# Optimization experiments

Hardware: AMD Instinct MI355X
Metric: run time of the kernel (lower is better)

## Reference

```python
import jax, jax.numpy as jnp
import numpy as np

N, D, E, H = 100000, 128, 1600000, 256  # nodes, feat dim, edges, backbone hidden
EPS = 1e-5
NEG_SLOPE = 0.01


def setup_inputs() -> dict:
    key = jax.random.key(0)
    ks = jax.random.split(key, 16)
    s = 0.02
    return {
        "x": jax.random.normal(ks[0], (N, D), dtype=jnp.float32),
        "edges": jax.random.randint(ks[1], (2, E), 0, N, dtype=jnp.int64),
        # merge layer: Linear(2D -> D)
        "W_merge": jax.random.normal(ks[2], (2 * D, D), dtype=jnp.float32) * s,
        "b_merge": jnp.zeros((D,), dtype=jnp.float32),
        # GRUCell(D, D): weights stored torch-style (3D, D)
        "W_ih": jax.random.normal(ks[3], (3 * D, D), dtype=jnp.float32) * s,
        "W_hh": jax.random.normal(ks[4], (3 * D, D), dtype=jnp.float32) * s,
        "b_ih": jnp.zeros((3 * D,), dtype=jnp.float32),
        "b_hh": jnp.zeros((3 * D,), dtype=jnp.float32),
        # backbone: Linear(D->256), BN(256), Linear(256->D), BN(D)
        "W1": jax.random.normal(ks[5], (D, H), dtype=jnp.float32) * s,
        "b1": jnp.zeros((H,), dtype=jnp.float32),
        "g1": jnp.ones((H,), dtype=jnp.float32),
        "be1": jnp.zeros((H,), dtype=jnp.float32),
        "W2": jax.random.normal(ks[6], (H, D), dtype=jnp.float32) * s,
        "b2": jnp.zeros((D,), dtype=jnp.float32),
        "g2": jnp.ones((D,), dtype=jnp.float32),
        "be2": jnp.zeros((D,), dtype=jnp.float32),
    }


def _batchnorm(y, g, b):
    m = jnp.mean(y, axis=0)
    v = jnp.var(y, axis=0)  # biased, as torch BN uses in normalization
    return g * (y - m) * jax.lax.rsqrt(v + EPS) + b


def _leaky_relu(y):
    return jnp.where(y >= 0, y, NEG_SLOPE * y)


def reference(x, edges, W_merge, b_merge, W_ih, W_hh, b_ih, b_hh,
              W1, b1, g1, be1, W2, b2, g2, be2):
    n = x.shape[0]
    src, dst = edges[0], edges[1]
    x_nbr = x[src]                                   # (E, D) gather
    agg_sum = jax.ops.segment_sum(x_nbr, dst, num_segments=n)
    agg_max = jax.ops.segment_max(x_nbr, dst, num_segments=n)
    agg_max = jnp.where(jnp.isneginf(agg_max), jnp.zeros_like(agg_max), agg_max)
    # merge 'cat' -> Linear(2D -> D)
    merged = jnp.concatenate([agg_sum, agg_max], axis=-1) @ W_merge + b_merge
    # GRUCell update: input=merged, hidden=x
    gi = merged @ W_ih.T + b_ih                      # (N, 3D)
    gh = x @ W_hh.T + b_hh                           # (N, 3D)
    i_r, i_z, i_n = jnp.split(gi, 3, axis=-1)
    h_r, h_z, h_n = jnp.split(gh, 3, axis=-1)
    r = jax.nn.sigmoid(i_r + h_r)
    z = jax.nn.sigmoid(i_z + h_z)
    nn_ = jnp.tanh(i_n + r * h_n)
    h = (1.0 - z) * nn_ + z * x
    # backbone
    y = _batchnorm(_leaky_relu(h @ W1 + b1), g1, be1)
    y = _batchnorm(_leaky_relu(y @ W2 + b2), g2, be2)
    return y
```

## Files before the change

### kernel.cpp

```cpp
#include <hip/hip_runtime.h>
#include <math.h>

#define DD 128
#define CAPB 2048
#define MAXNB 1600

typedef __attribute__((ext_vector_type(8))) short bf16x8;
typedef __attribute__((ext_vector_type(4))) float f32x4;

__device__ __forceinline__ unsigned short f2bf(float f) {
    unsigned u = __float_as_uint(f);
    unsigned r = u + 0x7FFF + ((u >> 16) & 1);
    return (unsigned short)(r >> 16);
}
__device__ __forceinline__ float bf2f(unsigned short h) {
    return __uint_as_float(((unsigned)h) << 16);
}

__device__ __forceinline__ float fsigm(float x) {
    float e = __builtin_amdgcn_exp2f(-1.442695041f * x);
    return __builtin_amdgcn_rcpf(1.0f + e);
}
__device__ __forceinline__ float ftanh(float x) {
    float e = __builtin_amdgcn_exp2f(2.885390082f * x);
    return 1.0f - 2.0f * __builtin_amdgcn_rcpf(1.0f + e);
}

__device__ __forceinline__ void gld16(const unsigned short* g, unsigned short* l) {
    __builtin_amdgcn_global_load_lds(
        (const __attribute__((address_space(1))) void*)g,
        (__attribute__((address_space(3))) void*)l, 16, 0, 0);
}

__global__ void k_wsfail(float* __restrict__ out, float val, int n) {
    int i = blockIdx.x * 256 + threadIdx.x;
    if (i < n) out[i] = (i == 0) ? val : 0.0f;
}

__global__ void k_setup(const int* __restrict__ e32, int* __restrict__ flag,
                        float* __restrict__ sums, int* __restrict__ gCur, int NB,
                        const float* __restrict__ W1, const float* __restrict__ W2,
                        unsigned short* __restrict__ w1T, unsigned short* __restrict__ w2T,
                        const float* __restrict__ x, unsigned short* __restrict__ AGG,
                        int total_x4) {
    const int bid = blockIdx.x;
    const int t = threadIdx.x;
    if (bid == 0) {
        if (t == 0) {
            int f = 1;
            for (int i = 1; i < 16; i += 2) f &= (e32[i] == 0);
            *flag = f;
        }
        for (int i = t; i < 768; i += 256) sums[i] = 0.0f;
    } else if (bid < 8) {
        int i = (bid - 1) * 256 + t;
        if (i < NB) gCur[i] = 0;
    } else if (bid < 136) {
        int i = (bid - 8) * 256 + t;
        int j = i >> 7, k = i & 127;
        w1T[j * 128 + k] = f2bf(W1[k * 256 + j]);
    } else if (bid < 264) {
        int i = (bid - 136) * 256 + t;
        int j = i >> 8, k = i & 255;
        w2T[j * 256 + k] = f2bf(W2[k * 128 + j]);
    } else {
        int idx = (bid - 264) * 256 + t;
        if (idx < total_x4) {
            int i = idx >> 5, j4 = (idx & 31) * 4;
            float4 v = *(const float4*)(x + (size_t)i * 128 + j4);
            unsigned lo = (unsigned)f2bf(v.x) | ((unsigned)f2bf(v.y) << 16);
            unsigned hi = (unsigned)f2bf(v.z) | ((unsigned)f2bf(v.w) << 16);
            unsigned short* p = AGG + (size_t)i * 384 + 256 + j4;
            *(unsigned*)(p) = lo;
            *(unsigned*)(p + 2) = hi;
        }
    }
}

__global__ void k_fusew(const float* __restrict__ Wm, const float* __restrict__ Wih,
                        const float* __restrict__ Whh, const float* __restrict__ bm,
                        const float* __restrict__ b_ih, const float* __restrict__ b_hh,
                        unsigned short* __restrict__ BtG, float* __restrict__ biasG) {
    const int j = blockIdx.x;
    const int c = threadIdx.x;
    const int g = j >> 7, d = j & 127;
    const int pj = ((d >> 4) << 6) + (g << 4) + (d & 15);
    float acc = 0.0f;
    if (j < 384) {
        const float* wr = Wih + (size_t)j * 128;
        const float* wc = Wm + (size_t)c * 128;
        for (int m = 0; m < 128; m++) acc += wc[m] * wr[m];
    }
    BtG[(size_t)pj * 384 + c] = f2bf(acc);
    if (c < 128) {
        float v = 0.0f;
        if (j < 256) v = Whh[(size_t)j * 128 + c];
        else if (j >= 384) v = Whh[(size_t)(j - 128) * 128 + c];
        BtG[(size_t)pj * 384 + 256 + c] = f2bf(v);
    }
    if (c == 0) {
        float b;
        if (j < 256) b = b_ih[j] + b_hh[j];
        else if (j < 384) b = b_ih[j];
        else b = b_hh[j - 128];
        if (j < 384) {
            const float* wr = Wih + (size_t)j * 128;
            float dd = 0.0f;
            for (int m = 0; m < 128; m++) dd += bm[m] * wr[m];
            b += dd;
        }
        biasG[pj] = b;
    }
}

__global__ __launch_bounds__(256) void k_bin(const void* __restrict__ edges_raw,
                                             const int* __restrict__ flag,
                                             int* __restrict__ gCur,
                                             unsigned* __restrict__ binned,
                                             int E, int Nn, int NB) {
    __shared__ int cnt_[MAXNB];
    __shared__ int cur_[MAXNB];
    const int t = threadIdx.x;
    const int e0 = blockIdx.x * 4096;
    for (int i = t; i < NB; i += 256) cnt_[i] = 0;
    __syncthreads();
    const int is64 = *flag;
    for (int k = 0; k < 16; k++) {
        int e = e0 + k * 256 + t;
        if (e < E) {
            int d = is64 ? (int)((const long long*)edges_raw)[(size_t)E + e]
                         : ((const int*)edges_raw)[(size_t)E + e];
            d = min(max(d, 0), Nn - 1);
            atomicAdd(&cnt_[d >> 6], 1);
        }
    }
    __syncthreads();
    for (int i = t; i < NB; i += 256) {
        int c = cnt_[i];
        cur_[i] = (c > 0) ? atomicAdd(&gCur[i], c) : 0;
    }
    __syncthreads();
    for (int k = 0; k < 16; k++) {
        int e = e0 + k * 256 + t;
        if (e < E) {
            int s, d;
            if (is64) {
                s = (int)((const long long*)edges_raw)[e];
                d = (int)((const long long*)edges_raw)[(size_t)E + e];
            } else {
                s = ((const int*)edges_raw)[e];
                d = ((const int*)edges_raw)[(size_t)E + e];
            }
            s = min(max(s, 0), Nn - 1);
            d = min(max(d, 0), Nn - 1);
            int b = d >> 6;
            int p = atomicAdd(&cur_[b], 1);
            if (p < CAPB)
                binned[(size_t)b * CAPB + p] = (unsigned)s | ((unsigned)(d & 63) << 23);
        }
    }
}

__global__ __launch_bounds__(256) void k_bagg(const unsigned* __restrict__ binned,
                                              const int* __restrict__ gCur,
                                              const void* __restrict__ edges_raw,
                                              const int* __restrict__ flag,
                                              unsigned short* __restrict__ AGG,
                                              int E, int Nn) {
    __shared__ unsigned lsrc[CAPB];
    __shared__ int deg_[64], off_[64], cur2_[64];
    __shared__ int sa[64], sb[64];
    const int t = threadIdx.x;
    const int wave = t >> 6;
    const int lane = t & 63;
    const int b = blockIdx.x;
    const int node0 = b << 6;
    const int nloc = min(64, Nn - node0);
    const int cnt = gCur[b];
    const int c2 = lane * 2;
    const unsigned c4 = (unsigned)lane * 4u;

    if (cnt <= CAPB) {
        if (t < 64) deg_[t] = 0;
        __syncthreads();
        for (int i = t; i < cnt; i += 256)
            atomicAdd(&deg_[binned[(size_t)b * CAPB + i] >> 23], 1);
        __syncthreads();
        if (t < 64) sa[t] = deg_[t];
        __syncthreads();
        for (int off = 1; off < 64; off <<= 1) {
            if (t < 64) sb[t] = sa[t] + ((t >= off) ? sa[t - off] : 0);
            __syncthreads();
            if (t < 64) sa[t] = sb[t];
            __syncthreads();
        }
        if (t < 64) {
            off_[t] = sa[t] - deg_[t];
            cur2_[t] = off_[t];
        }
        __syncthreads();
        for (int i = t; i < cnt; i += 256) {
            unsigned e = binned[(size_t)b * CAPB + i];
            int dl = e >> 23;
            int p = atomicAdd(&cur2_[dl], 1);
            lsrc[p] = (e & 0x7FFFFF) * 768u + 512u;
        }
        __syncthreads();
        const char* AGGb = (const char*)AGG;
        for (int ln = wave; ln < nloc; ln += 4) {
            const int o = off_[ln];
            const int d = deg_[ln];
            float sx = 0.f, sy = 0.f;
            float mx = -INFINITY, my = -INFINITY;
            int e = 0;
            for (; e + 7 < d; e += 8) {
                unsigned v[8];
#pragma unroll
                for (int u = 0; u < 8; u++)
                    v[u] = *(const unsigned*)(AGGb + lsrc[o + e + u] + c4);
#pragma unroll
                for (int u = 0; u < 8; u++) {
                    float lo = bf2f((unsigned short)(v[u] & 0xffff));
                    float hi = bf2f((unsigned short)(v[u] >> 16));
                    sx += lo; sy += hi;
                    mx = fmaxf(mx, lo); my = fmaxf(my, hi);
                }
            }
            for (; e + 3 < d; e += 4) {
                unsigned v[4];
#pragma unroll
                for (int u = 0; u < 4; u++)
                    v[u] = *(const unsigned*)(AGGb + lsrc[o + e + u] + c4);
#pragma unroll
                for (int u = 0; u < 4; u++) {
                    float lo = bf2f((unsigned short)(v[u] & 0xffff));
                    float hi = bf2f((unsigned short)(v[u] >> 16));
                    sx += lo; sy += hi;
                    mx = fmaxf(mx, lo); my = fmaxf(my, hi);
                }
            }
            for (; e < d; e++) {
                unsigned v0 = *(const unsigned*)(AGGb + lsrc[o + e] + c4);
                float lo = bf2f((unsigned short)(v0 & 0xffff));
                float hi = bf2f((unsigned short)(v0 >> 16));
                sx += lo; sy += hi;
                mx = fmaxf(mx, lo); my = fmaxf(my, hi);
            }
            if (d == 0) { mx = 0.f; my = 0.f; }
            unsigned short* row = AGG + (size_t)(node0 + ln) * 384;
            *(unsigned*)(row + c2) = (unsigned)f2bf(sx) | ((unsigned)f2bf(sy) << 16);
            *(unsigned*)(row + 128 + c2) = (unsigned)f2bf(mx) | ((unsigned)f2bf(my) << 16);
        }
    } else {
        const int is64 = *flag;
        for (int ln = wave; ln < nloc; ln += 4) {
            const int node = node0 + ln;
            float sx = 0.f, sy = 0.f;
            float mx = -INFINITY, my = -INFINITY;
            int d = 0;
            for (int e = 0; e < E; e++) {
                int dd = is64 ? (int)((const long long*)edges_raw)[(size_t)E + e]
                              : ((const int*)edges_raw)[(size_t)E + e];
                dd = min(max(dd, 0), Nn - 1);
                if (dd == node) {
                    int s = is64 ? (int)((const long long*)edges_raw)[e]
                                 : ((const int*)edges_raw)[e];
                    s = min(max(s, 0), Nn - 1);
                    unsigned v0 = *(const unsigned*)(AGG + (size_t)s * 384 + 256 + c2);
                    float ax = bf2f((unsigned short)(v0 & 0xffff));
                    float ay = bf2f((unsigned short)(v0 >> 16));
                    sx += ax; sy += ay;
                    mx = fmaxf(mx, ax); my = fmaxf(my, ay);
                    d++;
                }
            }
            if (d == 0) { mx = 0.f; my = 0.f; }
            unsigned short* row = AGG + (size_t)node * 384;
            *(unsigned*)(row + c2) = (unsigned)f2bf(sx) | ((unsigned)f2bf(sy) << 16);
            *(unsigned*)(row + 128 + c2) = (unsigned)f2bf(mx) | ((unsigned)f2bf(my) << 16);
        }
    }
}

template <int AFFINE, int LEAKY, int STATS, int GRUE>
__global__ __launch_bounds__(256) void k_mgemm(
    const unsigned short* __restrict__ A, int lda,
    const unsigned short* __restrict__ Bt,
    const float* __restrict__ bias,
    const float* __restrict__ sumA, const float* __restrict__ sqA,
    const float* __restrict__ gA, const float* __restrict__ beA,
    unsigned short* __restrict__ Cb, int ldc,
    int M, int K, float* __restrict__ sumO, float* __restrict__ sqO, float invN,
    const unsigned short* __restrict__ Xb) {
    __shared__ unsigned short ABs[2][2][4096];
    __shared__ float sc1[256], sh1[256];
    __shared__ float ssum[128], ssq[128];
    unsigned short* RP = &ABs[0][0][0];

    const int t = threadIdx.x;
    const int lane = t & 63;
    const int wave = t >> 6;
    const int wr = (wave >> 1) * 64;
    const int wc = (wave & 1) * 64;
    const int quad = lane >> 4;
    const int l16 = lane & 15;
    const int sig = (l16 >> 1) & 3;

    const int ncb = gridDim.x;
    const int nwg = ncb * gridDim.y;
    int lin = blockIdx.y * ncb + blockIdx.x;
    const int qq = nwg >> 3, rr = nwg & 7;
    const int xcd = lin & 7, pos = lin >> 3;
    const int nl = (xcd < rr ? xcd * (qq + 1) : rr * (qq + 1) + (xcd - rr) * qq) + pos;
    const int j0 = (nl % ncb) * 128;
    const int r0 = (nl / ncb) * 128;

    if (AFFINE) {
        float m = sumA[t] * invN;
        float v = sqA[t] * invN - m * m;
        if (v < 0.f) v = 0.f;
        float rs = rsqrtf(v + 1e-5f);
        float sc = gA[t] * rs;
        sc1[t] = sc;
        sh1[t] = beA[t] - m * sc;
    }
    if (STATS && t < 128) { ssum[t] = 0.f; ssq[t] = 0.f; }
    if (AFFINE || STATS) __syncthreads();

    f32x4 acc[4][4];
#pragma unroll
    for (int i = 0; i < 4; i++)
#pragma unroll
        for (int j = 0; j < 4; j++) acc[i][j] = (f32x4){0.f, 0.f, 0.f, 0.f};

    const int rowl = lane >> 2;
    const int gsw8 = (((lane & 3) ^ ((lane >> 3) & 3))) * 8;

    const int srow = t >> 2;
    const int sg8 = (t & 3) * 8;
    const int swz8 = (((t & 3) ^ ((t >> 3) & 3))) * 8;
    float4 areg[2];

    auto stageA = [&](int buf, int k0) {
#pragma unroll
        for (int p = 0; p < 2; p++) {
            int row = (wave * 2 + p) * 16 + rowl;
            int gr = r0 + row;
            if (gr >= M) gr = M - 1;
            gld16(A + (size_t)gr * lda + k0 + gsw8,
                  &ABs[buf][0][(wave * 2 + p) * 512]);
        }
    };
    auto stageB = [&](int buf, int k0) {
#pragma unroll
        for (int p = 0; p < 2; p++) {
            int row = (wave * 2 + p) * 16 + rowl;
            gld16(Bt + (size_t)(j0 + row) * K + k0 + gsw8,
                  &ABs[buf][1][(wave * 2 + p) * 512]);
        }
    };
    auto loadA = [&](int k0) {
#pragma unroll
        for (int p = 0; p < 2; p++) {
            int gr = r0 + p * 64 + srow;
            areg[p] = make_float4(0.f, 0.f, 0.f, 0.f);
            if (gr < M) areg[p] = *(const float4*)(A + (size_t)gr * lda + k0 + sg8);
        }
    };
    auto writeA = [&](int buf, int k0) {
        union U8 { float4 f; unsigned short u[8]; } uv;
#pragma unroll
        for (int p = 0; p < 2; p++) {
            uv.f = areg[p];
#pragma unroll
            for (int q = 0; q < 8; q++) {
                float f = bf2f(uv.u[q]) * sc1[k0 + sg8 + q] + sh1[k0 + sg8 + q];
                uv.u[q] = f2bf(f);
            }
            *(float4*)&ABs[buf][0][(p * 64 + srow) * 32 + swz8] = uv.f;
        }
    };

    if (!AFFINE) {
        stageA(0, 0); stageB(0, 0);
        if (32 < K) { stageA(1, 32); stageB(1, 32); }
        for (int k0 = 0; k0 < K; k0 += 32) {
            const int cur = (k0 >> 5) & 1;
            if (k0 + 32 < K)
                asm volatile("s_waitcnt vmcnt(4)\n\ts_barrier" ::: "memory");
            else
                asm volatile("s_waitcnt vmcnt(0)\n\ts_barrier" ::: "memory");
            bf16x8 af[4], bfr[4];
#pragma unroll
            for (int i = 0; i < 4; i++) {
                af[i]  = *(bf16x8*)&ABs[cur][0][(wr + i * 16 + l16) * 32 + (quad ^ sig) * 8];
                bfr[i] = *(bf16x8*)&ABs[cur][1][(wc + i * 16 + l16) * 32 + (quad ^ sig) * 8];
            }
            asm volatile("s_waitcnt lgkmcnt(0)\n\ts_barrier" ::: "memory");
            if (k0 + 64 < K) { stageA(cur, k0 + 64); stageB(cur, k0 + 64); }
#pragma unroll
            for (int mt = 0; mt < 4; mt++)
#pragma unroll
                for (int nt = 0; nt < 4; nt++)
                    acc[mt][nt] = __builtin_amdgcn_mfma_f32_16x16x32_bf16(
                        af[mt], bfr[nt], acc[mt][nt], 0, 0, 0);
        }
    } else {
        loadA(0); writeA(0, 0);
        stageB(0, 0);
        __syncthreads();
        int buf = 0;
        for (int k0 = 0; k0 < K; k0 += 32) {
            const int kn = k0 + 32;
            const bool hasNext = kn < K;
            if (hasNext) {
                loadA(kn);
                stageB(buf ^ 1, kn);
            }
            bf16x8 af[4], bfr[4];
#pragma unroll
            for (int i = 0; i < 4; i++) {
                af[i]  = *(bf16x8*)&ABs[buf][0][(wr + i * 16 + l16) * 32 + (quad ^ sig) * 8];
                bfr[i] = *(bf16x8*)&ABs[buf][1][(wc + i * 16 + l16) * 32 + (quad ^ sig) * 8];
            }
#pragma unroll
            for (int mt = 0; mt < 4; mt++)
#pragma unroll
                for (int nt = 0; nt < 4; nt++)
                    acc[mt][nt] = __builtin_amdgcn_mfma_f32_16x16x32_bf16(
                        af[mt], bfr[nt], acc[mt][nt], 0, 0, 0);
            if (hasNext) writeA(buf ^ 1, kn);
            __syncthreads();
            buf ^= 1;
        }
    }

    if (GRUE) {
        const int dimb = (j0 + wc) >> 2;
        const int dloc = (wc >> 2) + l16;
        const float bR = bias[j0 + wc + l16];
        const float bZ = bias[j0 + wc + 16 + l16];
        const float bI = bias[j0 + wc + 32 + l16];
        const float bH = bias[j0 + wc + 48 + l16];
#pragma unroll
        for (int mt = 0; mt < 4; mt++) {
#pragma unroll
            for (int reg = 0; reg < 4; reg++) {
                int rloc = wr + mt * 16 + quad * 4 + reg;
                int grow = r0 + rloc;
                int gi = grow < M ? grow : M - 1;
                float r = fsigm(acc[mt][0][reg] + bR);
                float z = fsigm(acc[mt][1][reg] + bZ);
                float nn = ftanh(acc[mt][2][reg] + bI + r * (acc[mt][3][reg] + bH));
                float xv = bf2f(Xb[(size_t)gi * 384 + 256 + dimb + l16]);
                float h = (1.0f - z) * nn + z * xv;
                RP[rloc * 40 + dloc] = f2bf(h);
            }
        }
        __syncthreads();
#pragma unroll
        for (int p = 0; p < 2; p++) {
            int id = p * 256 + t;
            int rloc = id >> 2, ck = id & 3;
            int grow = r0 + rloc;
            if (grow < M)
                *(float4*)(Cb + (size_t)grow * ldc + (j0 >> 2) + ck * 8) =
                    *(const float4*)&RP[rloc * 40 + ck * 8];
        }
        return;
    }

#pragma unroll
    for (int half = 0; half < 2; half++) {
        if (wr == half * 64) {
#pragma unroll
            for (int nt = 0; nt < 4; nt++) {
                int colLoc = wc + nt * 16 + l16;
                float bv = bias[j0 + colLoc];
                float s = 0.f, q = 0.f;
#pragma unroll
                for (int mt = 0; mt < 4; mt++) {
#pragma unroll
                    for (int reg = 0; reg < 4; reg++) {
                        int rloc = mt * 16 + quad * 4 + reg;
                        float v = acc[mt][nt][reg] + bv;
                        if (LEAKY) v = (v >= 0.f) ? v : 0.01f * v;
                        if (STATS && (r0 + half * 64 + rloc) < M) { s += v; q += v * v; }
                        RP[rloc * 128 + colLoc] = f2bf(v);
                    }
                }
                if (STATS) {
                    atomicAdd(&ssum[colLoc], s);
                    atomicAdd(&ssq[colLoc], q);
                }
            }
        }
        __syncthreads();
#pragma unroll
        for (int p = 0; p < 4; p++) {
            int id = p * 256 + t;
            int rloc = id >> 4;
            int ck = id & 15;
            int grow = r0 + half * 64 + rloc;
            if (grow < M)
                *(float4*)(Cb + (size_t)grow * ldc + j0 + ck * 8) =
                    *(const float4*)&RP[rloc * 128 + ck * 8];
        }
        __syncthreads();
    }
    if (STATS && t < 128) {
        atomicAdd(&sumO[j0 + t], ssum[t]);
        atomicAdd(&sqO[j0 + t], ssq[t]);
    }
}

__global__ void k_affine2(const unsigned short* __restrict__ ypre, float* __restrict__ out,
                          const float* __restrict__ sum2, const float* __restrict__ sq2,
                          const float* __restrict__ g2, const float* __restrict__ be2,
                          int total4, float invN) {
    __shared__ float sc[128], sh[128];
    int t = threadIdx.x;
    if (t < 128) {
        float m = sum2[t] * invN;
        float v = sq2[t] * invN - m * m;
        if (v < 0.f) v = 0.f;
        float rs = rsqrtf(v + 1e-5f);
        float s = g2[t] * rs;
        sc[t] = s;
        sh[t] = be2[t] - m * s;
    }
    __syncthreads();
    int idx = blockIdx.x * 256 + t;
    if (idx >= total4) return;
    int i4 = idx * 4;
    int c = i4 & 127;
    unsigned u0 = *(const unsigned*)(ypre + i4);
    unsigned u1 = *(const unsigned*)(ypre + i4 + 2);
    float4 o;
    o.x = bf2f((unsigned short)(u0 & 0xffff)) * sc[c]     + sh[c];
    o.y = bf2f((unsigned short)(u0 >> 16))    * sc[c + 1] + sh[c + 1];
    o.z = bf2f((unsigned short)(u1 & 0xffff)) * sc[c + 2] + sh[c + 2];
    o.w = bf2f((unsigned short)(u1 >> 16))    * sc[c + 3] + sh[c + 3];
    *(float4*)(out + i4) = o;
}

extern "C" void kernel_launch(void* const* d_in, const int* in_sizes, int n_in,
                              void* d_out, int out_size, void* d_ws, size_t ws_size,
                              hipStream_t stream) {
    const float* x       = (const float*)d_in[0];
    const void*  edges   = d_in[1];
    const float* W_merge = (const float*)d_in[2];
    const float* b_merge = (const float*)d_in[3];
    const float* W_ih    = (const float*)d_in[4];
    const float* W_hh    = (const float*)d_in[5];
    const float* b_ih    = (const float*)d_in[6];
    const float* b_hh    = (const float*)d_in[7];
    const float* W1      = (const float*)d_in[8];
    const float* b1      = (const float*)d_in[9];
    const float* g1      = (const float*)d_in[10];
    const float* be1     = (const float*)d_in[11];
    const float* W2      = (const float*)d_in[12];
    const float* b2      = (const float*)d_in[13];
    const float* g2      = (const float*)d_in[14];
    const float* be2     = (const float*)d_in[15];

    const int N = in_sizes[0] / DD;
    const int E = in_sizes[1] / 2;
    float* out = (float*)d_out;

    size_t need = ((size_t)640 * N + 120000) * sizeof(float);
    if (ws_size < need) {
        k_wsfail<<<(out_size + 255) / 256, 256, 0, stream>>>(
            out, (float)(ws_size >> 20), out_size);
        return;
    }

    const int NB = (N + 63) >> 6;

    float* ws = (float*)d_ws;
    unsigned short* AGG  = (unsigned short*)ws;
    unsigned short* y1b  = (unsigned short*)ws;
    unsigned short* ypre = (unsigned short*)(ws + (size_t)128 * N);
    unsigned short* hb16 = (unsigned short*)(ws + (size_t)448 * N);

    unsigned* binned = (unsigned*)(ws + (size_t)512 * N);
    int* gCur = (int*)(binned + (size_t)NB * CAPB);

    float* wbase = (float*)(gCur + NB + 64);
    unsigned short* BtG = (unsigned short*)wbase;
    unsigned short* w1T = (unsigned short*)(wbase + 98304);
    unsigned short* w2T = (unsigned short*)(wbase + 98304 + 16384);
    float* biasG = wbase + 98304 + 32768;
    float* sums  = biasG + 512;
    float* sum1 = sums, *sq1 = sums + 256, *sum2 = sums + 512, *sq2 = sums + 640;
    int*   flag  = (int*)(sums + 768);

    const int nrb  = (N + 127) / 128;
    const int ncvt4 = (N * 32 + 255) / 256;
    const float invN = 1.0f / (float)N;

    k_setup<<<264 + ncvt4, 256, 0, stream>>>(
        (const int*)edges, flag, sums, gCur, NB, W1, W2, w1T, w2T, x, AGG, N * 32);
    k_fusew<<<512, 256, 0, stream>>>(W_merge, W_ih, W_hh, b_merge, b_ih, b_hh, BtG, biasG);
    k_bin<<<(E + 4095) / 4096, 256, 0, stream>>>(edges, flag, gCur, binned, E, N, NB);
    k_bagg<<<NB, 256, 0, stream>>>(binned, gCur, edges, flag, AGG, E, N);
    k_mgemm<0, 0, 0, 1><<<dim3(4, nrb), 256, 0, stream>>>(
        AGG, 384, BtG, biasG, nullptr, nullptr, nullptr, nullptr,
        hb16, 128, N, 384, nullptr, nullptr, invN, AGG);
    k_mgemm<0, 1, 1, 0><<<dim3(2, nrb), 256, 0, stream>>>(
        hb16, 128, w1T, b1, nullptr, nullptr, nullptr, nullptr,
        y1b, 256, N, 128, sum1, sq1, invN, nullptr);
    k_mgemm<1, 1, 1, 0><<<dim3(1, nrb), 256, 0, stream>>>(
        y1b, 256, w2T, b2, sum1, sq1, g1, be1,
        ypre, 128, N, 256, sum2, sq2, invN, nullptr);
    k_affine2<<<ncvt4, 256, 0, stream>>>(ypre, out, sum2, sq2, g2, be2, N * 32, invN);
}
```

Before: 445.2 us.

## Split-edge 8-byte gathers in aggregation and dedicated 256-row GRU GEMM kernel

The aggregation kernel now has each half-wave handle alternating edges. Each lane loads 8 bytes (4 bf16 features), and the two halves are combined with a cross-half shuffle. The first half writes sums and the second half writes maxima. The fused merge/GRU GEMM moves out of the generic template into a dedicated kernel with 256-row tiles and 128 output columns per block. It uses direct-to-LDS async loads with double buffering, so each block covers two GRU dimension groups and reuses the B tile across more rows. The trade-off is higher register pressure (32 accumulators per wave) and fewer blocks, which may hurt occupancy.

```diff
diff --git a/kernel.cpp b/kernel.cpp
--- a/kernel.cpp
+++ b/kernel.cpp
@@ -177,8 +177,10 @@
     const int node0 = b << 6;
     const int nloc = min(64, Nn - node0);
     const int cnt = gCur[b];
+    const int half = lane >> 5;
+    const int hl = lane & 31;
+    const unsigned c8 = (unsigned)hl * 8u;
     const int c2 = lane * 2;
-    const unsigned c4 = (unsigned)lane * 4u;
 
     if (cnt <= CAPB) {
         if (t < 64) deg_[t] = 0;
@@ -210,46 +212,67 @@
         for (int ln = wave; ln < nloc; ln += 4) {
             const int o = off_[ln];
             const int d = deg_[ln];
-            float sx = 0.f, sy = 0.f;
-            float mx = -INFINITY, my = -INFINITY;
+            float s0 = 0.f, s1 = 0.f, s2 = 0.f, s3 = 0.f;
+            float m0 = -INFINITY, m1 = -INFINITY, m2 = -INFINITY, m3 = -INFINITY;
             int e = 0;
-            for (; e + 7 < d; e += 8) {
-                unsigned v[8];
+            for (; e + 15 < d; e += 16) {
+                uint2 v[8];
 #pragma unroll
                 for (int u = 0; u < 8; u++)
-                    v[u] = *(const unsigned*)(AGGb + lsrc[o + e + u] + c4);
+                    v[u] = *(const uint2*)(AGGb + lsrc[o + e + 2 * u + half] + c8);
 #pragma unroll
                 for (int u = 0; u < 8; u++) {
-                    float lo = bf2f((unsigned short)(v[u] & 0xffff));
-                    float hi = bf2f((unsigned short)(v[u] >> 16));
-                    sx += lo; sy += hi;
-                    mx = fmaxf(mx, lo); my = fmaxf(my, hi);
+                    float a = bf2f((unsigned short)(v[u].x & 0xffff));
+                    float bb = bf2f((unsigned short)(v[u].x >> 16));
+                    float cc = bf2f((unsigned short)(v[u].y & 0xffff));
+                    float dd2 = bf2f((unsigned short)(v[u].y >> 16));
+                    s0 += a; s1 += bb; s2 += cc; s3 += dd2;
+                    m0 = fmaxf(m0, a); m1 = fmaxf(m1, bb);
+                    m2 = fmaxf(m2, cc); m3 = fmaxf(m3, dd2);
                 }
             }
-            for (; e + 3 < d; e += 4) {
-                unsigned v[4];
-#pragma unroll
-                for (int u = 0; u < 4; u++)
-                    v[u] = *(const unsigned*)(AGGb + lsrc[o + e + u] + c4);
-#pragma unroll
-                for (int u = 0; u < 4; u++) {
-                    float lo = bf2f((unsigned short)(v[u] & 0xffff));
-                    float hi = bf2f((unsigned short)(v[u] >> 16));
-                    sx += lo; sy += hi;
-                    mx = fmaxf(mx, lo); my = fmaxf(my, hi);
+            for (; e + 1 < d; e += 2) {
+                uint2 v = *(const uint2*)(AGGb + lsrc[o + e + half] + c8);
+                float a = bf2f((unsigned short)(v.x & 0xffff));
+                float bb = bf2f((unsigned short)(v.x >> 16));
+                float cc = bf2f((unsigned short)(v.y & 0xffff));
+                float dd2 = bf2f((unsigned short)(v.y >> 16));
+                s0 += a; s1 += bb; s2 += cc; s3 += dd2;
+                m0 = fmaxf(m0, a); m1 = fmaxf(m1, bb);
+                m2 = fmaxf(m2, cc); m3 = fmaxf(m3, dd2);
+            }
+            if (e < d) {
+                uint2 v = *(const uint2*)(AGGb + lsrc[o + e] + c8);
+                float a = bf2f((unsigned short)(v.x & 0xffff));
+                float bb = bf2f((unsigned short)(v.x >> 16));
+                float cc = bf2f((unsigned short)(v.y & 0xffff));
+                float dd2 = bf2f((unsigned short)(v.y >> 16));
+                float ninf = -INFINITY;
+                if (half == 0) {
+                    s0 += a; s1 += bb; s2 += cc; s3 += dd2;
+                    m0 = fmaxf(m0, a); m1 = fmaxf(m1, bb);
+                    m2 = fmaxf(m2, cc); m3 = fmaxf(m3, dd2);
+                } else {
+                    m0 = fmaxf(m0, ninf);
                 }
             }
-            for (; e < d; e++) {
-                unsigned v0 = *(const unsigned*)(AGGb + lsrc[o + e] + c4);
-                float lo = bf2f((unsigned short)(v0 & 0xffff));
-                float hi = bf2f((unsigned short)(v0 >> 16));
-                sx += lo; sy += hi;
-                mx = fmaxf(mx, lo); my = fmaxf(my, hi);
-            }
-            if (d == 0) { mx = 0.f; my = 0.f; }
+            s0 += __shfl_xor(s0, 32); s1 += __shfl_xor(s1, 32);
+            s2 += __shfl_xor(s2, 32); s3 += __shfl_xor(s3, 32);
+            m0 = fmaxf(m0, __shfl_xor(m0, 32)); m1 = fmaxf(m1, __shfl_xor(m1, 32));
+            m2 = fmaxf(m2, __shfl_xor(m2, 32)); m3 = fmaxf(m3, __shfl_xor(m3, 32));
+            if (d == 0) { m0 = 0.f; m1 = 0.f; m2 = 0.f; m3 = 0.f; }
             unsigned short* row = AGG + (size_t)(node0 + ln) * 384;
-            *(unsigned*)(row + c2) = (unsigned)f2bf(sx) | ((unsigned)f2bf(sy) << 16);
-            *(unsigned*)(row + 128 + c2) = (unsigned)f2bf(mx) | ((unsigned)f2bf(my) << 16);
+            if (half == 0) {
+                uint2 sv;
+                sv.x = (unsigned)f2bf(s0) | ((unsigned)f2bf(s1) << 16);
+                sv.y = (unsigned)f2bf(s2) | ((unsigned)f2bf(s3) << 16);
+                *(uint2*)(row + 4 * hl) = sv;
+            } else {
+                uint2 mv;
+                mv.x = (unsigned)f2bf(m0) | ((unsigned)f2bf(m1) << 16);
+                mv.y = (unsigned)f2bf(m2) | ((unsigned)f2bf(m3) << 16);
+                *(uint2*)(row + 128 + 4 * hl) = mv;
+            }
         }
     } else {
         const int is64 = *flag;
@@ -282,7 +305,125 @@
     }
 }
 
-template <int AFFINE, int LEAKY, int STATS, int GRUE>
+__global__ __launch_bounds__(256) void k_gruemm(
+    const unsigned short* __restrict__ A,
+    const unsigned short* __restrict__ Bt,
+    const float* __restrict__ bias,
+    const unsigned short* __restrict__ Xb,
+    unsigned short* __restrict__ Cb,
+    int M) {
+    const int K = 384;
+    __shared__ unsigned short LD[2][12288];
+    unsigned short* RP = &LD[0][0];
+
+    const int t = threadIdx.x;
+    const int lane = t & 63;
+    const int wave = t >> 6;
+    const int quad = lane >> 4;
+    const int l16 = lane & 15;
+    const int sig = (l16 >> 1) & 3;
+    const int wr = wave * 64;
+
+    const int nwg = 4 * gridDim.y;
+    int lin = blockIdx.y * 4 + blockIdx.x;
+    const int qq = nwg >> 3, rr = nwg & 7;
+    const int xcd = lin & 7, pos = lin >> 3;
+    const int nl = (xcd < rr ? xcd * (qq + 1) : rr * (qq + 1) + (xcd - rr) * qq) + pos;
+    const int j0 = (nl & 3) * 128;
+    const int r0 = (nl >> 2) * 256;
+
+    f32x4 acc[4][8];
+#pragma unroll
+    for (int i = 0; i < 4; i++)
+#pragma unroll
+        for (int j = 0; j < 8; j++) acc[i][j] = (f32x4){0.f, 0.f, 0.f, 0.f};
+
+    const int rowl = lane >> 2;
+    const int gsw8 = (((lane & 3) ^ ((lane >> 3) & 3))) * 8;
+
+    auto stage = [&](int buf, int k0) {
+#pragma unroll
+        for (int p = 0; p < 4; p++) {
+            int row = (wave * 4 + p) * 16 + rowl;
+            int gr = r0 + row;
+            if (gr >= M) gr = M - 1;
+            gld16(A + (size_t)gr * 384 + k0 + gsw8,
+                  &LD[buf][(wave * 4 + p) * 512]);
+        }
+#pragma unroll
+        for (int p = 0; p < 2; p++) {
+            int row = (wave * 2 + p) * 16 + rowl;
+            gld16(Bt + (size_t)(j0 + row) * K + k0 + gsw8,
+                  &LD[buf][8192 + (wave * 2 + p) * 512]);
+        }
+    };
+
+    stage(0, 0);
+    stage(1, 32);
+    for (int k0 = 0; k0 < K; k0 += 32) {
+        const int cur = (k0 >> 5) & 1;
+        if (k0 + 32 < K)
+            asm volatile("s_waitcnt vmcnt(6)\n\ts_barrier" ::: "memory");
+        else
+            asm volatile("s_waitcnt vmcnt(0)\n\ts_barrier" ::: "memory");
+        bf16x8 af[4], bfr[8];
+#pragma unroll
+        for (int i = 0; i < 4; i++)
+            af[i] = *(bf16x8*)&LD[cur][(wr + i * 16 + l16) * 32 + (quad ^ sig) * 8];
+#pragma unroll
+        for (int i = 0; i < 8; i++)
+            bfr[i] = *(bf16x8*)&LD[cur][8192 + (i * 16 + l16) * 32 + (quad ^ sig) * 8];
+        asm volatile("s_waitcnt lgkmcnt(0)\n\ts_barrier" ::: "memory");
+        if (k0 + 64 < K) stage(cur, k0 + 64);
+#pragma unroll
+        for (int mt = 0; mt < 4; mt++)
+#pragma unroll
+            for (int nt = 0; nt < 8; nt++)
+                acc[mt][nt] = __builtin_amdgcn_mfma_f32_16x16x32_bf16(
+                    af[mt], bfr[nt], acc[mt][nt], 0, 0, 0);
+    }
+
+    const int dimb = j0 >> 2;
+    float bR[2], bZ[2], bI[2], bH[2];
+#pragma unroll
+    for (int dh = 0; dh < 2; dh++) {
+        bR[dh] = bias[j0 + dh * 64 + l16];
+        bZ[dh] = bias[j0 + dh * 64 + 16 + l16];
+        bI[dh] = bias[j0 + dh * 64 + 32 + l16];
+        bH[dh] = bias[j0 + dh * 64 + 48 + l16];
+    }
+#pragma unroll
+    for (int mt = 0; mt < 4; mt++) {
+#pragma unroll
+        for (int reg = 0; reg < 4; reg++) {
+            int rloc = wr + mt * 16 + quad * 4 + reg;
+            int grow = r0 + rloc;
+            int gi = grow < M ? grow : M - 1;
+#pragma unroll
+            for (int dh = 0; dh < 2; dh++) {
+                float r = fsigm(acc[mt][dh * 4 + 0][reg] + bR[dh]);
+                float z = fsigm(acc[mt][dh * 4 + 1][reg] + bZ[dh]);
+                float nn = ftanh(acc[mt][dh * 4 + 2][reg] + bI[dh] +
+                                 r * (acc[mt][dh * 4 + 3][reg] + bH[dh]));
+                float xv = bf2f(Xb[(size_t)gi * 384 + 256 + dimb + dh * 16 + l16]);
+                float h = (1.0f - z) * nn + z * xv;
+                RP[rloc * 40 + dh * 16 + l16] = f2bf(h);
+            }
+        }
+    }
+    __syncthreads();
+#pragma unroll
+    for (int p = 0; p < 4; p++) {
+        int id = p * 256 + t;
+        int rloc = id >> 2, ck = id & 3;
+        int grow = r0 + rloc;
+        if (grow < M)
+            *(float4*)(Cb + (size_t)grow * 128 + dimb + ck * 8) =
+                *(const float4*)&RP[rloc * 40 + ck * 8];
+    }
+}
+
+template <int AFFINE, int LEAKY, int STATS>
 __global__ __launch_bounds__(256) void k_mgemm(
     const unsigned short* __restrict__ A, int lda,
     const unsigned short* __restrict__ Bt,
@@ -290,8 +431,7 @@
     const float* __restrict__ sumA, const float* __restrict__ sqA,
     const float* __restrict__ gA, const float* __restrict__ beA,
     unsigned short* __restrict__ Cb, int ldc,
-    int M, int K, float* __restrict__ sumO, float* __restrict__ sqO, float invN,
-    const unsigned short* __restrict__ Xb) {
+    int M, int K, float* __restrict__ sumO, float* __restrict__ sqO, float invN) {
     __shared__ unsigned short ABs[2][2][4096];
     __shared__ float sc1[256], sh1[256];
     __shared__ float ssum[128], ssq[128];
@@ -433,41 +573,6 @@
             __syncthreads();
             buf ^= 1;
         }
-    }
-
-    if (GRUE) {
-        const int dimb = (j0 + wc) >> 2;
-        const int dloc = (wc >> 2) + l16;
-        const float bR = bias[j0 + wc + l16];
-        const float bZ = bias[j0 + wc + 16 + l16];
-        const float bI = bias[j0 + wc + 32 + l16];
-        const float bH = bias[j0 + wc + 48 + l16];
-#pragma unroll
-        for (int mt = 0; mt < 4; mt++) {
-#pragma unroll
-            for (int reg = 0; reg < 4; reg++) {
-                int rloc = wr + mt * 16 + quad * 4 + reg;
-                int grow = r0 + rloc;
-                int gi = grow < M ? grow : M - 1;
-                float r = fsigm(acc[mt][0][reg] + bR);
-                float z = fsigm(acc[mt][1][reg] + bZ);
-                float nn = ftanh(acc[mt][2][reg] + bI + r * (acc[mt][3][reg] + bH));
-                float xv = bf2f(Xb[(size_t)gi * 384 + 256 + dimb + l16]);
-                float h = (1.0f - z) * nn + z * xv;
-                RP[rloc * 40 + dloc] = f2bf(h);
-            }
-        }
-        __syncthreads();
-#pragma unroll
-        for (int p = 0; p < 2; p++) {
-            int id = p * 256 + t;
-            int rloc = id >> 2, ck = id & 3;
-            int grow = r0 + rloc;
-            if (grow < M)
-                *(float4*)(Cb + (size_t)grow * ldc + (j0 >> 2) + ck * 8) =
-                    *(const float4*)&RP[rloc * 40 + ck * 8];
-        }
-        return;
     }
 
 #pragma unroll
@@ -596,6 +701,7 @@
     int*   flag  = (int*)(sums + 768);
 
     const int nrb  = (N + 127) / 128;
+    const int nrb2 = (N + 255) / 256;
     const int ncvt4 = (N * 32 + 255) / 256;
     const float invN = 1.0f / (float)N;
 
@@ -604,14 +710,12 @@
     k_fusew<<<512, 256, 0, stream>>>(W_merge, W_ih, W_hh, b_merge, b_ih, b_hh, BtG, biasG);
     k_bin<<<(E + 4095) / 4096, 256, 0, stream>>>(edges, flag, gCur, binned, E, N, NB);
     k_bagg<<<NB, 256, 0, stream>>>(binned, gCur, edges, flag, AGG, E, N);
-    k_mgemm<0, 0, 0, 1><<<dim3(4, nrb), 256, 0, stream>>>(
-        AGG, 384, BtG, biasG, nullptr, nullptr, nullptr, nullptr,
-        hb16, 128, N, 384, nullptr, nullptr, invN, AGG);
-    k_mgemm<0, 1, 1, 0><<<dim3(2, nrb), 256, 0, stream>>>(
+    k_gruemm<<<dim3(4, nrb2), 256, 0, stream>>>(AGG, BtG, biasG, AGG, hb16, N);
+    k_mgemm<0, 1, 1><<<dim3(2, nrb), 256, 0, stream>>>(
         hb16, 128, w1T, b1, nullptr, nullptr, nullptr, nullptr,
-        y1b, 256, N, 128, sum1, sq1, invN, nullptr);
-    k_mgemm<1, 1, 1, 0><<<dim3(1, nrb), 256, 0, stream>>>(
+        y1b, 256, N, 128, sum1, sq1, invN);
+    k_mgemm<1, 1, 1><<<dim3(1, nrb), 256, 0, stream>>>(
         y1b, 256, w2T, b2, sum1, sq1, g1, be1,
-        ypre, 128, N, 256, sum2, sq2, invN, nullptr);
+        ypre, 128, N, 256, sum2, sq2, invN);
     k_affine2<<<ncvt4, 256, 0, stream>>>(ypre, out, sum2, sq2, g2, be2, N * 32, invN);
 }
```

Result: slower. 464.0 us (+4.2%).
